# Kernel optimization log

Measured on AMD Instinct MI355X. Metric: run time of the kernel, lower is better.

## Reference

```python
import jax, jax.numpy as jnp
import numpy as np

N, D = 16384, 2048


def setup_inputs() -> dict:
    key = jax.random.key(0)
    k1, k2 = jax.random.split(key)
    x = jax.random.normal(k1, (N, D), dtype=jnp.float32)
    mask = jax.random.randint(k2, (N, D), 0, 2) > 0
    return {"x": x, "mask": mask}


def _masked_sparsemax(z, m):
    """Project each row of z onto the simplex restricted to positions where m is True.

    Fully batched equivalent of the TF per-row map_fn/cond/boolean_mask version.
    z: [..., D] float, m: [..., D] bool. Returns p with p>=0, sum over active = 1
    (all-zeros row if no active entries).
    """
    d = z.shape[-1]
    num_active = jnp.sum(m, axis=-1, keepdims=True)                 # [..., 1] int
    # Masked entries sort to the tail (-inf), so the first num_active sorted
    # entries are exactly the active values in descending order.
    z_neg = jnp.where(m, z, -jnp.inf)
    z_sorted = -jnp.sort(-z_neg, axis=-1)                           # descending
    k_int = jnp.arange(1, d + 1)
    k = k_int.astype(z.dtype)
    active_pos = k_int <= num_active                                # [..., D]
    # cumsum over active sorted entries only (zeros beyond num_active)
    csum = jnp.cumsum(jnp.where(active_pos, z_sorted, 0.0), axis=-1)
    # support condition: z_(k) - (csum_k - 1)/k > 0  <=>  k*z_(k) > csum_k - 1
    cond = (z_sorted * k > (csum - 1.0)) & active_pos
    rho = jnp.sum(cond, axis=-1, keepdims=True)                     # support size
    rho_idx = jnp.clip(rho - 1, 0, d - 1)
    csum_rho = jnp.take_along_axis(csum, rho_idx, axis=-1)
    theta = (csum_rho - 1.0) / jnp.maximum(rho, 1).astype(z.dtype)
    p_valid = jnp.maximum(z - theta, 0.0)
    # TF invalid_branch fallback: uniform over active entries (unreachable in
    # exact arithmetic since k=1 always satisfies cond, kept for faithfulness)
    p_uniform = 1.0 / jnp.maximum(num_active, 1).astype(z.dtype)
    p = jnp.where(rho > 0, p_valid, p_uniform)
    return jnp.where(m & (num_active > 0), p, 0.0)


def reference(x, mask):
    # axis = -1: project along the last axis (the TF layer transposes the
    # chosen axis to last; with axis=-1 that transpose is the identity).
    return _masked_sparsemax(x, mask)
```

## Files before the change

kernel.cpp:

```cpp
#include <hip/hip_runtime.h>
#include <math.h>


constexpr int D   = 2048;
constexpr int TPB = 256;
constexpr int EPT = D / TPB;

__global__ __launch_bounds__(TPB) void sparsemax_kernel(
    const float* __restrict__ x,
    const int*   __restrict__ mask,
    float*       __restrict__ out)
{
    const int    row  = blockIdx.x;
    const int    t    = threadIdx.x;
    const size_t base = (size_t)row * D + (size_t)t * EPT;

    float4 a  = ((const float4*)(x    + base))[0];
    float4 b  = ((const float4*)(x    + base))[1];
    int4   ma = ((const int4*)  (mask + base))[0];
    int4   mb = ((const int4*)  (mask + base))[1];

    float z[EPT];
    z[0] = ma.x ? a.x : -INFINITY;
    z[1] = ma.y ? a.y : -INFINITY;
    z[2] = ma.z ? a.z : -INFINITY;
    z[3] = ma.w ? a.w : -INFINITY;
    z[4] = mb.x ? b.x : -INFINITY;
    z[5] = mb.y ? b.y : -INFINITY;
    z[6] = mb.z ? b.z : -INFINITY;
    z[7] = mb.w ? b.w : -INFINITY;

    __shared__ float s_red[8];
    __shared__ float s_bc[2];

    float theta = -INFINITY;
    float prevC = -1.0f;

    for (int it = 0; it < 128; ++it) {
        float ps = 0.0f, pc = 0.0f;
        #pragma unroll
        for (int k = 0; k < EPT; ++k) {
            if (z[k] > theta) { ps += z[k]; pc += 1.0f; }
        }
        #pragma unroll
        for (int off = 32; off > 0; off >>= 1) {
            ps += __shfl_down(ps, off, 64);
            pc += __shfl_down(pc, off, 64);
        }
        const int wid = t >> 6;
        if ((t & 63) == 0) { s_red[wid] = ps; s_red[4 + wid] = pc; }
        __syncthreads();
        if (t == 0) {
            s_bc[0] = s_red[0] + s_red[1] + s_red[2] + s_red[3];
            s_bc[1] = s_red[4] + s_red[5] + s_red[6] + s_red[7];
        }
        __syncthreads();
        const float S = s_bc[0];
        const float C = s_bc[1];
        if (C == 0.0f) { theta = INFINITY; break; }
        if (C == prevC) break;
        theta = (S - 1.0f) / C;
        prevC = C;
    }

    float4 o0, o1;
    o0.x = fmaxf(z[0] - theta, 0.0f);
    o0.y = fmaxf(z[1] - theta, 0.0f);
    o0.z = fmaxf(z[2] - theta, 0.0f);
    o0.w = fmaxf(z[3] - theta, 0.0f);
    o1.x = fmaxf(z[4] - theta, 0.0f);
    o1.y = fmaxf(z[5] - theta, 0.0f);
    o1.z = fmaxf(z[6] - theta, 0.0f);
    o1.w = fmaxf(z[7] - theta, 0.0f);
    ((float4*)(out + base))[0] = o0;
    ((float4*)(out + base))[1] = o1;
}

extern "C" void kernel_launch(void* const* d_in, const int* in_sizes, int n_in,
                              void* d_out, int out_size, void* d_ws, size_t ws_size,
                              hipStream_t stream) {
    const float* x    = (const float*)d_in[0];
    const int*   mask = (const int*)  d_in[1];
    float*       out  = (float*)d_out;
    const int n_rows = in_sizes[0] / D;
    sparsemax_kernel<<<n_rows, TPB, 0, stream>>>(x, mask, out);
}
```

Measured before the change: 315.4 us.

## Map one wavefront per row and use ballot-based counts in the sparsemax iteration

New measurement: 330.7 us. 1.05x slower.

```diff
diff --git a/kernel.cpp b/kernel.cpp
--- a/kernel.cpp
+++ b/kernel.cpp
@@ -2,78 +2,79 @@
 #include <math.h>
 
 
-constexpr int D   = 2048;
-constexpr int TPB = 256;
-constexpr int EPT = D / TPB;
+constexpr int D     = 2048;
+constexpr int LANES = 64;
+constexpr int EPT   = D / LANES;
+constexpr int RPB   = 4;
+constexpr int TPB   = RPB * LANES;
 
 __global__ __launch_bounds__(TPB) void sparsemax_kernel(
     const float* __restrict__ x,
     const int*   __restrict__ mask,
     float*       __restrict__ out)
 {
-    const int    row  = blockIdx.x;
-    const int    t    = threadIdx.x;
-    const size_t base = (size_t)row * D + (size_t)t * EPT;
-
-    float4 a  = ((const float4*)(x    + base))[0];
-    float4 b  = ((const float4*)(x    + base))[1];
-    int4   ma = ((const int4*)  (mask + base))[0];
-    int4   mb = ((const int4*)  (mask + base))[1];
+    const int    wid  = threadIdx.x >> 6;
+    const int    lane = threadIdx.x & 63;
+    const size_t row  = (size_t)blockIdx.x * RPB + wid;
+    const size_t base = row * D + (size_t)lane * EPT;
 
     float z[EPT];
-    z[0] = ma.x ? a.x : -INFINITY;
-    z[1] = ma.y ? a.y : -INFINITY;
-    z[2] = ma.z ? a.z : -INFINITY;
-    z[3] = ma.w ? a.w : -INFINITY;
-    z[4] = mb.x ? b.x : -INFINITY;
-    z[5] = mb.y ? b.y : -INFINITY;
-    z[6] = mb.z ? b.z : -INFINITY;
-    z[7] = mb.w ? b.w : -INFINITY;
+    float S = 0.0f;
+    int   C = 0;
+    #pragma unroll
+    for (int i = 0; i < EPT / 4; ++i) {
+        const float4 a = ((const float4*)(x    + base))[i];
+        const int4   m = ((const int4*)  (mask + base))[i];
+        z[4*i + 0] = m.x ? a.x : -INFINITY;
+        z[4*i + 1] = m.y ? a.y : -INFINITY;
+        z[4*i + 2] = m.z ? a.z : -INFINITY;
+        z[4*i + 3] = m.w ? a.w : -INFINITY;
+        S += m.x ? a.x : 0.0f;
+        S += m.y ? a.y : 0.0f;
+        S += m.z ? a.z : 0.0f;
+        S += m.w ? a.w : 0.0f;
+        C += __popcll(__ballot(m.x != 0));
+        C += __popcll(__ballot(m.y != 0));
+        C += __popcll(__ballot(m.z != 0));
+        C += __popcll(__ballot(m.w != 0));
+    }
+    #pragma unroll
+    for (int off = 32; off > 0; off >>= 1)
+        S += __shfl_xor(S, off, 64);
 
-    __shared__ float s_red[8];
-    __shared__ float s_bc[2];
-
-    float theta = -INFINITY;
-    float prevC = -1.0f;
-
-    for (int it = 0; it < 128; ++it) {
-        float ps = 0.0f, pc = 0.0f;
-        #pragma unroll
-        for (int k = 0; k < EPT; ++k) {
-            if (z[k] > theta) { ps += z[k]; pc += 1.0f; }
+    float theta;
+    if (C == 0) {
+        theta = INFINITY;
+    } else {
+        theta = (S - 1.0f) / (float)C;
+        int prevC = C;
+        for (int it = 0; it < 64; ++it) {
+            float s = 0.0f;
+            int   c = 0;
+            #pragma unroll
+            for (int k = 0; k < EPT; ++k) {
+                const float d = z[k] - theta;
+                s += fmaxf(d, 0.0f);
+                c += __popcll(__ballot(d > 0.0f));
+            }
+            if (c == prevC) break;
+            #pragma unroll
+            for (int off = 32; off > 0; off >>= 1)
+                s += __shfl_xor(s, off, 64);
+            theta += (s - 1.0f) / (float)c;
+            prevC = c;
         }
-        #pragma unroll
-        for (int off = 32; off > 0; off >>= 1) {
-            ps += __shfl_down(ps, off, 64);
-            pc += __shfl_down(pc, off, 64);
-        }
-        const int wid = t >> 6;
-        if ((t & 63) == 0) { s_red[wid] = ps; s_red[4 + wid] = pc; }
-        __syncthreads();
-        if (t == 0) {
-            s_bc[0] = s_red[0] + s_red[1] + s_red[2] + s_red[3];
-            s_bc[1] = s_red[4] + s_red[5] + s_red[6] + s_red[7];
-        }
-        __syncthreads();
-        const float S = s_bc[0];
-        const float C = s_bc[1];
-        if (C == 0.0f) { theta = INFINITY; break; }
-        if (C == prevC) break;
-        theta = (S - 1.0f) / C;
-        prevC = C;
     }
 
-    float4 o0, o1;
-    o0.x = fmaxf(z[0] - theta, 0.0f);
-    o0.y = fmaxf(z[1] - theta, 0.0f);
-    o0.z = fmaxf(z[2] - theta, 0.0f);
-    o0.w = fmaxf(z[3] - theta, 0.0f);
-    o1.x = fmaxf(z[4] - theta, 0.0f);
-    o1.y = fmaxf(z[5] - theta, 0.0f);
-    o1.z = fmaxf(z[6] - theta, 0.0f);
-    o1.w = fmaxf(z[7] - theta, 0.0f);
-    ((float4*)(out + base))[0] = o0;
-    ((float4*)(out + base))[1] = o1;
+    #pragma unroll
+    for (int i = 0; i < EPT / 4; ++i) {
+        float4 o;
+        o.x = fmaxf(z[4*i + 0] - theta, 0.0f);
+        o.y = fmaxf(z[4*i + 1] - theta, 0.0f);
+        o.z = fmaxf(z[4*i + 2] - theta, 0.0f);
+        o.w = fmaxf(z[4*i + 3] - theta, 0.0f);
+        ((float4*)(out + base))[i] = o;
+    }
 }
 
 extern "C" void kernel_launch(void* const* d_in, const int* in_sizes, int n_in,
@@ -83,5 +84,5 @@
     const int*   mask = (const int*)  d_in[1];
     float*       out  = (float*)d_out;
     const int n_rows = in_sizes[0] / D;
-    sparsemax_kernel<<<n_rows, TPB, 0, stream>>>(x, mask, out);
+    sparsemax_kernel<<<n_rows / RPB, TPB, 0, stream>>>(x, mask, out);
 }
```
